# Kernel tuning notes

Measured on AMD Instinct MI355X. Metric: run time of the kernel, lower is better.

The kernel has to match this reference:

```python
import jax, jax.numpy as jnp
import numpy as np

B, N, C = 32, 64, 128   # events, particles/event, channels (hidden==hidden2==out)
NUM_MAPS = 15           # bell_number(2+2)
E = B * N * N
LN_EPS = 1e-5


def setup_inputs() -> dict:
    key = jax.random.key(0)
    ks = jax.random.split(key, 8)
    x = jax.random.normal(ks[0], (E, C), jnp.float32)
    # complete graph with self-loops per event, nodes of event b are b*N..b*N+N-1
    node = np.arange(B * N, dtype=np.int32).reshape(B, N)
    src = np.repeat(node, N, axis=1).reshape(-1)            # i index per edge
    dst = np.tile(node, (1, N)).reshape(-1)                 # j index per edge
    edge_index = jnp.asarray(np.stack([src, dst]), jnp.int32)
    batch = jnp.asarray(np.repeat(np.arange(B, dtype=np.int32), N))
    # params: Linear(C->C), LayerNorm(C), factorized aggregator coeffs
    W_in = jax.random.normal(ks[1], (C, C), jnp.float32) / np.sqrt(C)
    b_in = jnp.zeros((C,), jnp.float32)
    ln_g = jnp.ones((C,), jnp.float32)
    ln_b = jnp.zeros((C,), jnp.float32)
    s0 = np.sqrt(3.0 / NUM_MAPS)
    s1 = np.sqrt(3.0 / C)
    c00 = jax.random.uniform(ks[2], (C, NUM_MAPS), jnp.float32, -s0, s0)
    c01 = jax.random.uniform(ks[3], (C, NUM_MAPS), jnp.float32, -s0, s0)
    c10 = jax.random.uniform(ks[4], (C, C), jnp.float32, -s1, s1)
    c11 = jax.random.uniform(ks[5], (C, C), jnp.float32, -s1, s1)
    return {"x": x, "edge_index": edge_index, "batch": batch,
            "W_in": W_in, "b_in": b_in, "ln_g": ln_g, "ln_b": ln_b,
            "c00": c00, "c01": c01, "c10": c10, "c11": c11}


def reference(x, edge_index, batch, W_in, b_in, ln_g, ln_b, c00, c01, c10, c11):
    # mlp: Linear -> GELU -> LayerNorm (this order, per ModuleList)
    h = x @ W_in.T + b_in
    h = jax.nn.gelu(h, approximate=False)
    mu = h.mean(-1, keepdims=True)
    var = ((h - mu) ** 2).mean(-1, keepdims=True)
    h = (h - mu) / jnp.sqrt(var + LN_EPS) * ln_g + ln_b

    # aggregate_2to2 with reduce='mean': 15 Eq(2->2) permutation-equivariant maps.
    # edge_index/batch describe complete graphs of N nodes per event -> dense view.
    t = h.reshape(B, N, N, C)                 # t[b,i,j,c]
    row = t.mean(axis=2)                      # [B,N,C] mean_j t[b,i,j]
    col = t.mean(axis=1)                      # [B,N,C] mean_i t[b,i,j]
    idx = jnp.arange(N)
    diag = t[:, idx, idx]                     # [B,N,C]
    trace = diag.mean(axis=1)                 # [B,C]
    tot = t.mean(axis=(1, 2))                 # [B,C]
    eye = jnp.eye(N, dtype=t.dtype)[None, :, :, None]

    # factorized coeffs [C_in?, C_out?, 15]; with C_in==C_out the flatten/linear in
    # the torch code makes the FIRST axis the output channel: out = sum map_m @ coeffs[:,:,m].T
    coeffs = c00[:, None, :] * c10[:, :, None] + c01[None, :, :] * c11[:, :, None]

    def proj(a, m):  # a[..., c] -> [..., o] with W[o, c] = coeffs[o, c, m]
        return jnp.einsum('...c,oc->...o', a, coeffs[:, :, m])

    out = proj(t, 0) + proj(t.swapaxes(1, 2), 1)
    out = out + proj(diag, 2)[:, :, None, :] + proj(diag, 3)[:, None, :, :]
    out = out + proj(row, 4)[:, :, None, :] + proj(row, 5)[:, None, :, :]
    out = out + proj(col, 6)[:, :, None, :] + proj(col, 7)[:, None, :, :]
    out = out + proj(trace, 8)[:, None, None, :] + proj(tot, 9)[:, None, None, :]
    out = out + eye * (proj(diag, 10)[:, :, None, :]
                       + proj(row, 11)[:, :, None, :]
                       + proj(col, 12)[:, :, None, :])
    out = out + eye * (proj(trace, 13)[:, None, None, :]
                       + proj(tot, 14)[:, None, None, :])

    return jax.nn.gelu(out.reshape(E, C), approximate=False)
```

## Files before the change

kernel.cpp:

```cpp
#include <hip/hip_runtime.h>
#include <hip/hip_bf16.h>


#define B_ 32
#define N_ 64
#define C_ 128
#define E_ (B_ * N_ * N_)
#define LN_EPS 1e-5f

typedef unsigned int u32;
typedef unsigned short u16;
typedef short bf16x8 __attribute__((ext_vector_type(8)));
typedef float f32x16 __attribute__((ext_vector_type(16)));

union FragU { uint4 u; bf16x8 v; };

__device__ inline float bf_u16(u16 u) { return __uint_as_float(((u32)u) << 16); }
__device__ inline u32 pack_bf2(float a, float b) {
    __hip_bfloat16 ha = __float2bfloat16(a), hb = __float2bfloat16(b);
    u16 ra = *reinterpret_cast<u16*>(&ha), rb = *reinterpret_cast<u16*>(&hb);
    return (u32)ra | ((u32)rb << 16);
}
__device__ inline u16 pack_bf1(float a) {
    __hip_bfloat16 ha = __float2bfloat16(a);
    return *reinterpret_cast<u16*>(&ha);
}
__device__ inline float b2f(__hip_bfloat16 v) { return __bfloat162float(v); }
__device__ inline float geluf(float v) {
    float v2 = v * v;
    float w = fmaf(0.044715f * v2, v, v);
    float e = __builtin_amdgcn_exp2f(2.3022083f * w);
    return v - v * __builtin_amdgcn_rcpf(e + 1.0f);
}
__device__ inline float ld1(const void* p, int i, int isbf) {
    if (isbf) return b2f(((const __hip_bfloat16*)p)[i]);
    return ((const float*)p)[i];
}
__device__ inline int bf_flag(const void* gp) {
    return (((const u32*)gp)[0] == 0x3F803F80u) ? 1 : 0;
}

#define O_T      ((size_t)0)
#define O_ROW    ((size_t)33554432)
#define O_DIAG   ((size_t)35651584)
#define O_CT     ((size_t)36732928)
#define O_WF     ((size_t)37715968)
#define O_CF     ((size_t)37748736)
#define O_U      ((size_t)37912576)
#define O_V      ((size_t)38961152)
#define O_DGN    ((size_t)40026112)

__global__ void pack_all(const void* __restrict__ W,
                         const void* __restrict__ c00, const void* __restrict__ c01,
                         const void* __restrict__ c10, const void* __restrict__ c11,
                         const void* __restrict__ gp,
                         uint4* __restrict__ WF, uint4* __restrict__ CF,
                         float* __restrict__ cT) {
    int isbf = bf_flag(gp);
    if (blockIdx.x < 24) {
        int idx = blockIdx.x * 256 + threadIdx.x;
        if (idx < 2048) {
            int l = idx & 63, s = (idx >> 6) & 7, ot = idx >> 9;
            int n = ot * 32 + (l & 31), k0 = s * 16 + (l >> 5) * 8;
            float v[8];
#pragma unroll
            for (int j = 0; j < 8; ++j) v[j] = ld1(W, n * 128 + k0 + j, isbf);
            uint4 o;
            o.x = pack_bf2(v[0], v[1]); o.y = pack_bf2(v[2], v[3]);
            o.z = pack_bf2(v[4], v[5]); o.w = pack_bf2(v[6], v[7]);
            WF[(s * 4 + ot) * 64 + l] = o;
        } else {
            int id2 = idx - 2048;
            int mat = id2 >> 11, r = id2 & 2047;
            int l = r & 63, s = (r >> 6) & 7, ot = r >> 9;
            int n = ot * 32 + (l & 31), k0 = s * 16 + (l >> 5) * 8;
            float v[8];
#pragma unroll
            for (int j = 0; j < 8; ++j) {
                int k = k0 + j;
                v[j] = ld1(c00, n * 15 + mat, isbf) * ld1(c10, n * 128 + k, isbf) +
                       ld1(c01, k * 15 + mat, isbf) * ld1(c11, n * 128 + k, isbf);
            }
            uint4 o;
            o.x = pack_bf2(v[0], v[1]); o.y = pack_bf2(v[2], v[3]);
            o.z = pack_bf2(v[4], v[5]); o.w = pack_bf2(v[6], v[7]);
            CF[mat * 2048 + (s * 4 + ot) * 64 + l] = o;
        }
    } else {
        int idx2 = (blockIdx.x - 24) * 256 + threadIdx.x;
        int m = idx2 >> 14, rem = idx2 & 16383;
        int c = rem >> 7, o = rem & 127;
        float val = ld1(c00, o * 15 + m, isbf) * ld1(c10, o * 128 + c, isbf) +
                    ld1(c01, c * 15 + m, isbf) * ld1(c11, o * 128 + c, isbf);
        cT[(m * 128 + c) * 128 + o] = val;
    }
}

__global__ void __launch_bounds__(256, 4) gemm_ln_mfma(const void* __restrict__ x,
                                                       const uint4* __restrict__ WF,
                                                       const void* __restrict__ bp, const void* __restrict__ gp,
                                                       const void* __restrict__ lbp,
                                                       u16* __restrict__ t,
                                                       float* __restrict__ row_sum, float* __restrict__ diag) {
    __shared__ __align__(16) float fbuf[64 * 128];
    __shared__ float st[64][2];
    __shared__ float rsbuf[2][128];
    u16* atile = (u16*)fbuf;
    int tid = threadIdx.x;
    int w = tid >> 6, l = tid & 63;
    int wr = w >> 1, wc = w & 1;
    int m = l & 31, hh = l >> 5;
    int isbf = bf_flag(gp);
    int e0 = blockIdx.x * 64;
    int b = e0 >> 12, i = (e0 >> 6) & 63;

    FragU bfr[16];
#pragma unroll
    for (int s = 0; s < 8; ++s)
#pragma unroll
        for (int ot = 0; ot < 2; ++ot)
            bfr[s * 2 + ot].u = WF[(s * 4 + wc * 2 + ot) * 64 + l];

#pragma unroll
    for (int q = 0; q < 4; ++q) {
        int c = q * 256 + tid;
        int row = c >> 4, c16 = c & 15;
        int sw = (c16 * 16) ^ ((row & 15) << 4);
        uint4 val;
        if (isbf) {
            val = *(const uint4*)((const u16*)x + (size_t)(e0 + row) * 128 + c16 * 8);
        } else {
            const float* xf = (const float*)x + (size_t)(e0 + row) * 128 + c16 * 8;
            float4 f0 = *(const float4*)xf;
            float4 f1 = *(const float4*)(xf + 4);
            val.x = pack_bf2(f0.x, f0.y); val.y = pack_bf2(f0.z, f0.w);
            val.z = pack_bf2(f1.x, f1.y); val.w = pack_bf2(f1.z, f1.w);
        }
        *(uint4*)((char*)atile + row * 256 + sw) = val;
    }
    __syncthreads();

    f32x16 acc[2];
#pragma unroll
    for (int ot = 0; ot < 2; ++ot)
#pragma unroll
        for (int r = 0; r < 16; ++r) acc[ot][r] = 0.f;

    int arow = wr * 32 + m;
    const char* abase = (const char*)atile + arow * 256;
    int amask = (arow & 15) << 4;
#pragma unroll
    for (int s = 0; s < 8; ++s) {
        FragU af;
        af.u = *(const uint4*)(abase + ((s * 32 + hh * 16) ^ amask));
        acc[0] = __builtin_amdgcn_mfma_f32_32x32x16_bf16(af.v, bfr[s * 2 + 0].v, acc[0], 0, 0, 0);
        acc[1] = __builtin_amdgcn_mfma_f32_32x32x16_bf16(af.v, bfr[s * 2 + 1].v, acc[1], 0, 0, 0);
    }

    int o0 = wc * 64 + m, o1 = o0 + 32;
    float bias0 = ld1(bp, o0, isbf), bias1 = ld1(bp, o1, isbf);
    float g0 = ld1(gp, o0, isbf), g1 = ld1(gp, o1, isbf);
    float bo0 = ld1(lbp, o0, isbf), bo1 = ld1(lbp, o1, isbf);

#pragma unroll
    for (int r = 0; r < 16; ++r) {
        acc[0][r] = geluf(acc[0][r] + bias0);
        acc[1][r] = geluf(acc[1][r] + bias1);
    }
    __syncthreads();

#pragma unroll
    for (int r = 0; r < 16; ++r) {
        int j = wr * 32 + (r & 3) + 8 * (r >> 2) + 4 * hh;
        fbuf[j * 128 + o0] = acc[0][r];
        fbuf[j * 128 + o1] = acc[1][r];
    }
    __syncthreads();

    {
        int j2 = tid >> 2, q = tid & 3;
        const float* rp = fbuf + j2 * 128 + q * 32;
        float s = 0.f, s2 = 0.f;
#pragma unroll
        for (int k = 0; k < 32; ++k) {
            float v = rp[k];
            s += v;
            s2 = fmaf(v, v, s2);
        }
        s += __shfl_xor(s, 1); s2 += __shfl_xor(s2, 1);
        s += __shfl_xor(s, 2); s2 += __shfl_xor(s2, 2);
        if (q == 0) {
            float mean = s * (1.0f / 128.0f);
            float var = s2 * (1.0f / 128.0f) - mean * mean;
            st[j2][0] = mean;
            st[j2][1] = rsqrtf(var + LN_EPS);
        }
    }
    __syncthreads();

    u16* tls = atile;
    float rsum0 = 0.f, rsum1 = 0.f;
    int ni = b * 64 + i;
#pragma unroll
    for (int r = 0; r < 16; ++r) {
        int j = wr * 32 + (r & 3) + 8 * (r >> 2) + 4 * hh;
        float mean = st[j][0], rstd = st[j][1];
        float y0 = (acc[0][r] - mean) * rstd * g0 + bo0;
        float y1 = (acc[1][r] - mean) * rstd * g1 + bo1;
        rsum0 += y0; rsum1 += y1;
        tls[j * 128 + o0] = pack_bf1(y0);
        tls[j * 128 + o1] = pack_bf1(y1);
        if (j == i) {
            diag[(size_t)ni * 128 + o0] = y0;
            diag[(size_t)ni * 128 + o1] = y1;
        }
    }
    rsum0 += __shfl_xor(rsum0, 32);
    rsum1 += __shfl_xor(rsum1, 32);
    if (l < 32) { rsbuf[wr][o0] = rsum0; rsbuf[wr][o1] = rsum1; }
    __syncthreads();

    if (tid < 128) row_sum[(size_t)ni * 128 + tid] = rsbuf[0][tid] + rsbuf[1][tid];
#pragma unroll
    for (int q = 0; q < 4; ++q) {
        int c = q * 256 + tid;
        *(uint4*)&t[(size_t)e0 * 128 + c * 8] = *(const uint4*)&tls[c * 8];
    }
}

__global__ void __launch_bounds__(512) uvall_kernel(const u16* __restrict__ t,
                                                    const float* __restrict__ row_sum,
                                                    const float* __restrict__ diag,
                                                    const float* __restrict__ cT,
                                                    float* __restrict__ U, float* __restrict__ V,
                                                    float* __restrict__ DgN) {
    __shared__ float dg[4][128], rm[4][128], cm[4][128];
    __shared__ float trs[128], tts[128];
    __shared__ float pU[4][4][128], pV[4][4][128], pD[4][4][128];
    __shared__ float paw[4][128], pad_[4][128];
    int b = blockIdx.x >> 4, n0 = (blockIdx.x & 15) * 4;
    int tid = threadIdx.x;
    int o = tid & 127, cq = tid >> 7;

    {
        int g = (b * 64 + n0 + cq) * 128 + o;
        dg[cq][o] = diag[g];
        rm[cq][o] = row_sum[g] * (1.0f / 64.0f);
    }
    float cs[4];
#pragma unroll
    for (int nn = 0; nn < 4; ++nn) {
        size_t base = (((size_t)(b << 12) + (n0 + nn)) << 7) + o + ((size_t)cq << 17);
        float s = 0.f;
#pragma unroll
        for (int i = 0; i < 16; ++i) s += bf_u16(t[base + ((size_t)i << 13)]);
        cs[nn] = s;
    }
    float tr = 0.f, tt = 0.f;
#pragma unroll
    for (int n = 0; n < 16; ++n) {
        int g = (b * 64 + cq * 16 + n) * 128 + o;
        tr += diag[g];
        tt += row_sum[g];
    }
#pragma unroll
    for (int nn = 0; nn < 4; ++nn) pU[cq][nn][o] = cs[nn];
    paw[cq][o] = tr;
    pad_[cq][o] = tt;
    __syncthreads();
    cm[cq][o] = (pU[0][cq][o] + pU[1][cq][o] + pU[2][cq][o] + pU[3][cq][o]) * (1.0f / 64.0f);
    if (cq == 0) trs[o] = (paw[0][o] + paw[1][o] + paw[2][o] + paw[3][o]) * (1.0f / 64.0f);
    if (cq == 1) tts[o] = (pad_[0][o] + pad_[1][o] + pad_[2][o] + pad_[3][o]) * (1.0f / 4096.0f);
    __syncthreads();

    float aU[4] = {0}, aV[4] = {0}, aD[4] = {0}, aw = 0.f, ad = 0.f;
    int c0 = cq * 32;
    for (int cc = 0; cc < 32; ++cc) {
        int c = c0 + cc;
        float c2 = cT[(2 * 128 + c) * 128 + o], c4 = cT[(4 * 128 + c) * 128 + o], c6 = cT[(6 * 128 + c) * 128 + o];
        float c3 = cT[(3 * 128 + c) * 128 + o], c5 = cT[(5 * 128 + c) * 128 + o], c7 = cT[(7 * 128 + c) * 128 + o];
        float cA = cT[(10 * 128 + c) * 128 + o], cB = cT[(11 * 128 + c) * 128 + o], cC = cT[(12 * 128 + c) * 128 + o];
        float c8 = cT[(8 * 128 + c) * 128 + o], c9 = cT[(9 * 128 + c) * 128 + o];
        float cD = cT[(13 * 128 + c) * 128 + o], cE = cT[(14 * 128 + c) * 128 + o];
        float trv = trs[c], ttv = tts[c];
        aw += c8 * trv + c9 * ttv;
        ad += cD * trv + cE * ttv;
#pragma unroll
        for (int nn = 0; nn < 4; ++nn) {
            float d = dg[nn][c], r = rm[nn][c], cl = cm[nn][c];
            aU[nn] += c2 * d + c4 * r + c6 * cl;
            aV[nn] += c3 * d + c5 * r + c7 * cl;
            aD[nn] += cA * d + cB * r + cC * cl;
        }
    }
#pragma unroll
    for (int nn = 0; nn < 4; ++nn) {
        pU[cq][nn][o] = aU[nn];
        pV[cq][nn][o] = aV[nn];
        pD[cq][nn][o] = aD[nn];
    }
    paw[cq][o] = aw;
    pad_[cq][o] = ad;
    __syncthreads();
    {
        int nn = cq;
        float u = pU[0][nn][o] + pU[1][nn][o] + pU[2][nn][o] + pU[3][nn][o];
        float v = pV[0][nn][o] + pV[1][nn][o] + pV[2][nn][o] + pV[3][nn][o];
        float d = pD[0][nn][o] + pD[1][nn][o] + pD[2][nn][o] + pD[3][nn][o];
        float w = paw[0][o] + paw[1][o] + paw[2][o] + paw[3][o];
        float a = pad_[0][o] + pad_[1][o] + pad_[2][o] + pad_[3][o];
        int g = (b * 64 + n0 + nn) * 128 + o;
        U[g] = u + w;
        V[g] = v;
        DgN[g] = d + a;
    }
}

__global__ void __launch_bounds__(256) final_mfma(const u16* __restrict__ t,
                                                  const uint4* __restrict__ CF,
                                                  const float* __restrict__ U, const float* __restrict__ V,
                                                  const float* __restrict__ DgN, const void* __restrict__ gp,
                                                  void* __restrict__ outp) {
    __shared__ __align__(16) uint4 cfl[2048];
    u16* ols = (u16*)cfl;
    int w = threadIdx.x >> 6, l = threadIdx.x & 63;
    int m = l & 31, hh = l >> 5;
    int e0 = blockIdx.x * 128;
    int b = e0 >> 12;
    int i0 = (e0 >> 6) & 63;
    int iw = i0 + (w >> 1);
    int jA = (w & 1) * 32 + m;
    const u16* ai_base = t + (size_t)(e0 + w * 32 + m) * 128;
    const u16* aj_base = t + (size_t)((b << 12) + (jA << 6) + iw) * 128;

#pragma unroll
    for (int k = 0; k < 8; ++k) {
        int idx = k * 256 + threadIdx.x;
        cfl[idx] = CF[idx];
    }

    FragU af[8], ag[8];
#pragma unroll
    for (int s = 0; s < 8; ++s) {
        int k0 = s * 16 + hh * 8;
        af[s].u = *(const uint4*)(ai_base + k0);
        ag[s].u = *(const uint4*)(aj_base + k0);
    }
    __syncthreads();

    f32x16 acc[4];
#pragma unroll
    for (int ot = 0; ot < 4; ++ot)
#pragma unroll
        for (int r = 0; r < 16; ++r) acc[ot][r] = 0.f;

#pragma unroll
    for (int s = 0; s < 8; ++s) {
#pragma unroll
        for (int ot = 0; ot < 4; ++ot) {
            FragU b0;
            b0.u = cfl[(s * 4 + ot) * 64 + l];
            acc[ot] = __builtin_amdgcn_mfma_f32_32x32x16_bf16(af[s].v, b0.v, acc[ot], 0, 0, 0);
        }
    }
    __syncthreads();
#pragma unroll
    for (int k = 0; k < 8; ++k) {
        int idx = k * 256 + threadIdx.x;
        cfl[idx] = CF[2048 + idx];
    }
    __syncthreads();
#pragma unroll
    for (int s = 0; s < 8; ++s) {
#pragma unroll
        for (int ot = 0; ot < 4; ++ot) {
            FragU b1;
            b1.u = cfl[(s * 4 + ot) * 64 + l];
            acc[ot] = __builtin_amdgcn_mfma_f32_32x32x16_bf16(ag[s].v, b1.v, acc[ot], 0, 0, 0);
        }
    }

    int ni = b * 64 + iw;
    int isbf = bf_flag(gp);
    float uw[4], dg4[4];
#pragma unroll
    for (int ot = 0; ot < 4; ++ot) {
        int o = ot * 32 + m;
        uw[ot] = U[ni * 128 + o];
        dg4[ot] = DgN[ni * 128 + o];
    }
    if (isbf) {
        __syncthreads();
#pragma unroll
        for (int r = 0; r < 16; ++r) {
            int row = (r & 3) + 8 * (r >> 2) + 4 * hh;
            int jD = (w & 1) * 32 + row;
            int nj = b * 64 + jD;
            bool dia = (jD == iw);
#pragma unroll
            for (int ot = 0; ot < 4; ++ot) {
                int o = ot * 32 + m;
                float val = acc[ot][r] + uw[ot] + V[nj * 128 + o];
                if (dia) val += dg4[ot];
                ols[(w * 32 + row) * 128 + o] = pack_bf1(geluf(val));
            }
        }
        __syncthreads();
        u16* ob = (u16*)outp;
#pragma unroll
        for (int q = 0; q < 8; ++q) {
            int chunk = q * 256 + threadIdx.x;
            int row = chunk >> 4, c16 = chunk & 15;
            uint4 v = *(const uint4*)&ols[row * 128 + c16 * 8];
            *(uint4*)&ob[(e0 + row) * 128 + c16 * 8] = v;
        }
    } else {
        float* ob = (float*)outp;
#pragma unroll
        for (int r = 0; r < 16; ++r) {
            int row = (r & 3) + 8 * (r >> 2) + 4 * hh;
            int jD = (w & 1) * 32 + row;
            int e = e0 + w * 32 + row;
            int nj = b * 64 + jD;
            bool dia = (jD == iw);
#pragma unroll
            for (int ot = 0; ot < 4; ++ot) {
                int o = ot * 32 + m;
                float val = acc[ot][r] + uw[ot] + V[nj * 128 + o];
                if (dia) val += dg4[ot];
                ob[e * 128 + o] = geluf(val);
            }
        }
    }
}

extern "C" void kernel_launch(void* const* d_in, const int* in_sizes, int n_in,
                              void* d_out, int out_size, void* d_ws, size_t ws_size,
                              hipStream_t stream) {
    const void* x = d_in[0];
    const void* W = d_in[3];
    const void* bp = d_in[4];
    const void* gp = d_in[5];
    const void* lbp = d_in[6];
    const void* c00 = d_in[7];
    const void* c01 = d_in[8];
    const void* c10 = d_in[9];
    const void* c11 = d_in[10];

    char* ws = (char*)d_ws;
    u16* t16 = (u16*)(ws + O_T);
    float* row_sum = (float*)(ws + O_ROW);
    float* diag = (float*)(ws + O_DIAG);
    float* cT = (float*)(ws + O_CT);
    uint4* WF = (uint4*)(ws + O_WF);
    uint4* CF = (uint4*)(ws + O_CF);
    float* Uarr = (float*)(ws + O_U);
    float* Varr = (float*)(ws + O_V);
    float* DgN = (float*)(ws + O_DGN);

    pack_all<<<984, 256, 0, stream>>>(W, c00, c01, c10, c11, gp, WF, CF, cT);
    gemm_ln_mfma<<<E_ / 64, 256, 0, stream>>>(x, WF, bp, gp, lbp, t16, row_sum, diag);
    uvall_kernel<<<B_ * 16, 512, 0, stream>>>(t16, row_sum, diag, cT, Uarr, Varr, DgN);
    final_mfma<<<E_ / 128, 256, 0, stream>>>(t16, CF, Uarr, Varr, DgN, gp, (void*)d_out);
}
```

Measured before the change: 195.5 us.

## Retile final MFMA kernel to one row per block, loading coeff fragments directly

The final kernel now processes 64 edges (one i row) per block instead of 128, with waves split across j-halves and output-channel halves. Each wave keeps 2 accumulators instead of 4. Coefficient fragments are read straight from global memory into registers, which removes the LDS staging and its barriers. This raises grid size and occupancy (launch bounds 3). In exchange each block re-reads the coefficient matrix from global/L2 with less reuse per block.

Measured after the change: 204.8 us. 4.8% more time.

```diff
diff --git a/kernel.cpp b/kernel.cpp
--- a/kernel.cpp
+++ b/kernel.cpp
@@ -316,120 +316,94 @@
     }
 }
 
-__global__ void __launch_bounds__(256) final_mfma(const u16* __restrict__ t,
-                                                  const uint4* __restrict__ CF,
-                                                  const float* __restrict__ U, const float* __restrict__ V,
-                                                  const float* __restrict__ DgN, const void* __restrict__ gp,
-                                                  void* __restrict__ outp) {
-    __shared__ __align__(16) uint4 cfl[2048];
-    u16* ols = (u16*)cfl;
-    int w = threadIdx.x >> 6, l = threadIdx.x & 63;
+__global__ void __launch_bounds__(256, 3) final_mfma(const u16* __restrict__ t,
+                                                     const uint4* __restrict__ CF,
+                                                     const float* __restrict__ U, const float* __restrict__ V,
+                                                     const float* __restrict__ DgN, const void* __restrict__ gp,
+                                                     void* __restrict__ outp) {
+    __shared__ __align__(16) u16 ols[64 * 128];
+    int tid = threadIdx.x;
+    int w = tid >> 6, l = tid & 63;
+    int wr = w >> 1, wc = w & 1;
     int m = l & 31, hh = l >> 5;
-    int e0 = blockIdx.x * 128;
-    int b = e0 >> 12;
-    int i0 = (e0 >> 6) & 63;
-    int iw = i0 + (w >> 1);
-    int jA = (w & 1) * 32 + m;
-    const u16* ai_base = t + (size_t)(e0 + w * 32 + m) * 128;
-    const u16* aj_base = t + (size_t)((b << 12) + (jA << 6) + iw) * 128;
-
-#pragma unroll
-    for (int k = 0; k < 8; ++k) {
-        int idx = k * 256 + threadIdx.x;
-        cfl[idx] = CF[idx];
-    }
-
-    FragU af[8], ag[8];
-#pragma unroll
-    for (int s = 0; s < 8; ++s) {
-        int k0 = s * 16 + hh * 8;
-        af[s].u = *(const uint4*)(ai_base + k0);
-        ag[s].u = *(const uint4*)(aj_base + k0);
-    }
-    __syncthreads();
-
-    f32x16 acc[4];
-#pragma unroll
-    for (int ot = 0; ot < 4; ++ot)
+    int e0 = blockIdx.x * 64;
+    int b = e0 >> 12, i = (e0 >> 6) & 63;
+    int isbf = bf_flag(gp);
+
+    const u16* ai_base = t + (size_t)(e0 + wr * 32 + m) * 128;
+    const u16* aj_base = t + (size_t)((b << 12) + ((wr * 32 + m) << 6) + i) * 128;
+
+    f32x16 acc[2];
+#pragma unroll
+    for (int ot = 0; ot < 2; ++ot)
 #pragma unroll
         for (int r = 0; r < 16; ++r) acc[ot][r] = 0.f;
 
-#pragma unroll
-    for (int s = 0; s < 8; ++s) {
-#pragma unroll
-        for (int ot = 0; ot < 4; ++ot) {
-            FragU b0;
-            b0.u = cfl[(s * 4 + ot) * 64 + l];
-            acc[ot] = __builtin_amdgcn_mfma_f32_32x32x16_bf16(af[s].v, b0.v, acc[ot], 0, 0, 0);
-        }
-    }
-    __syncthreads();
-#pragma unroll
-    for (int k = 0; k < 8; ++k) {
-        int idx = k * 256 + threadIdx.x;
-        cfl[idx] = CF[2048 + idx];
-    }
-    __syncthreads();
-#pragma unroll
-    for (int s = 0; s < 8; ++s) {
-#pragma unroll
-        for (int ot = 0; ot < 4; ++ot) {
-            FragU b1;
-            b1.u = cfl[(s * 4 + ot) * 64 + l];
-            acc[ot] = __builtin_amdgcn_mfma_f32_32x32x16_bf16(ag[s].v, b1.v, acc[ot], 0, 0, 0);
-        }
-    }
-
-    int ni = b * 64 + iw;
-    int isbf = bf_flag(gp);
-    float uw[4], dg4[4];
-#pragma unroll
-    for (int ot = 0; ot < 4; ++ot) {
-        int o = ot * 32 + m;
-        uw[ot] = U[ni * 128 + o];
-        dg4[ot] = DgN[ni * 128 + o];
-    }
+    {
+        FragU bc[16], af[8];
+#pragma unroll
+        for (int s = 0; s < 8; ++s) {
+            bc[s * 2 + 0].u = CF[(s * 4 + wc * 2 + 0) * 64 + l];
+            bc[s * 2 + 1].u = CF[(s * 4 + wc * 2 + 1) * 64 + l];
+            af[s].u = *(const uint4*)(ai_base + s * 16 + hh * 8);
+        }
+#pragma unroll
+        for (int s = 0; s < 8; ++s) {
+            acc[0] = __builtin_amdgcn_mfma_f32_32x32x16_bf16(af[s].v, bc[s * 2 + 0].v, acc[0], 0, 0, 0);
+            acc[1] = __builtin_amdgcn_mfma_f32_32x32x16_bf16(af[s].v, bc[s * 2 + 1].v, acc[1], 0, 0, 0);
+        }
+    }
+    {
+        FragU bc[16], af[8];
+#pragma unroll
+        for (int s = 0; s < 8; ++s) {
+            bc[s * 2 + 0].u = CF[2048 + (s * 4 + wc * 2 + 0) * 64 + l];
+            bc[s * 2 + 1].u = CF[2048 + (s * 4 + wc * 2 + 1) * 64 + l];
+            af[s].u = *(const uint4*)(aj_base + s * 16 + hh * 8);
+        }
+#pragma unroll
+        for (int s = 0; s < 8; ++s) {
+            acc[0] = __builtin_amdgcn_mfma_f32_32x32x16_bf16(af[s].v, bc[s * 2 + 0].v, acc[0], 0, 0, 0);
+            acc[1] = __builtin_amdgcn_mfma_f32_32x32x16_bf16(af[s].v, bc[s * 2 + 1].v, acc[1], 0, 0, 0);
+        }
+    }
+
+    int o0 = wc * 64 + m, o1 = o0 + 32;
+    int ni = b * 64 + i;
+    float uw0 = U[(size_t)ni * 128 + o0], uw1 = U[(size_t)ni * 128 + o1];
+    float dg0 = DgN[(size_t)ni * 128 + o0], dg1 = DgN[(size_t)ni * 128 + o1];
+
     if (isbf) {
-        __syncthreads();
 #pragma unroll
         for (int r = 0; r < 16; ++r) {
             int row = (r & 3) + 8 * (r >> 2) + 4 * hh;
-            int jD = (w & 1) * 32 + row;
-            int nj = b * 64 + jD;
-            bool dia = (jD == iw);
-#pragma unroll
-            for (int ot = 0; ot < 4; ++ot) {
-                int o = ot * 32 + m;
-                float val = acc[ot][r] + uw[ot] + V[nj * 128 + o];
-                if (dia) val += dg4[ot];
-                ols[(w * 32 + row) * 128 + o] = pack_bf1(geluf(val));
-            }
+            int j = wr * 32 + row;
+            int nj = b * 64 + j;
+            float v0 = acc[0][r] + uw0 + V[(size_t)nj * 128 + o0];
+            float v1 = acc[1][r] + uw1 + V[(size_t)nj * 128 + o1];
+            if (j == i) { v0 += dg0; v1 += dg1; }
+            ols[j * 128 + o0] = pack_bf1(geluf(v0));
+            ols[j * 128 + o1] = pack_bf1(geluf(v1));
         }
         __syncthreads();
         u16* ob = (u16*)outp;
 #pragma unroll
-        for (int q = 0; q < 8; ++q) {
-            int chunk = q * 256 + threadIdx.x;
-            int row = chunk >> 4, c16 = chunk & 15;
-            uint4 v = *(const uint4*)&ols[row * 128 + c16 * 8];
-            *(uint4*)&ob[(e0 + row) * 128 + c16 * 8] = v;
+        for (int q = 0; q < 4; ++q) {
+            int c = q * 256 + tid;
+            *(uint4*)&ob[(size_t)e0 * 128 + c * 8] = *(const uint4*)&ols[c * 8];
         }
     } else {
         float* ob = (float*)outp;
 #pragma unroll
         for (int r = 0; r < 16; ++r) {
             int row = (r & 3) + 8 * (r >> 2) + 4 * hh;
-            int jD = (w & 1) * 32 + row;
-            int e = e0 + w * 32 + row;
-            int nj = b * 64 + jD;
-            bool dia = (jD == iw);
-#pragma unroll
-            for (int ot = 0; ot < 4; ++ot) {
-                int o = ot * 32 + m;
-                float val = acc[ot][r] + uw[ot] + V[nj * 128 + o];
-                if (dia) val += dg4[ot];
-                ob[e * 128 + o] = geluf(val);
-            }
+            int j = wr * 32 + row;
+            int nj = b * 64 + j;
+            float v0 = acc[0][r] + uw0 + V[(size_t)nj * 128 + o0];
+            float v1 = acc[1][r] + uw1 + V[(size_t)nj * 128 + o1];
+            if (j == i) { v0 += dg0; v1 += dg1; }
+            ob[(size_t)(e0 + j) * 128 + o0] = geluf(v0);
+            ob[(size_t)(e0 + j) * 128 + o1] = geluf(v1);
         }
     }
 }
@@ -461,5 +435,5 @@
     pack_all<<<984, 256, 0, stream>>>(W, c00, c01, c10, c11, gp, WF, CF, cT);
     gemm_ln_mfma<<<E_ / 64, 256, 0, stream>>>(x, WF, bp, gp, lbp, t16, row_sum, diag);
     uvall_kernel<<<B_ * 16, 512, 0, stream>>>(t16, row_sum, diag, cT, Uarr, Varr, DgN);
-    final_mfma<<<E_ / 128, 256, 0, stream>>>(t16, CF, Uarr, Varr, DgN, gp, (void*)d_out);
-}
+    final_mfma<<<E_ / 64, 256, 0, stream>>>(t16, CF, Uarr, Varr, DgN, gp, (void*)d_out);
+}
```
